# Performance work log

Hardware: AMD Instinct MI355X
Metric: run time of the kernel (lower is better)

The kernel has to match this reference:

```python
import jax, jax.numpy as jnp
import numpy as np

B, C, H, W = 2, 256, 80, 160
G, P, E = 8, 8, 2  # groups(heads), sampling points, ffn expansion
LN_EPS = 1e-5


def setup_inputs() -> dict:
    key = jax.random.key(0)
    ks = jax.random.split(key, 12)
    def n(k, shape, s=1.0):
        return jax.random.normal(k, shape, dtype=jnp.float32) * s
    return dict(
        feats=n(ks[0], (B, C, H, W)),
        feats_pos=n(ks[1], (B, C, H, W)),
        anchor_points=jax.random.uniform(ks[2], (B, H, W, 2), dtype=jnp.float32),
        value_W=n(ks[3], (C, C), 0.02), value_b=jnp.zeros((C,), jnp.float32),
        off_W=n(ks[4], (C, G * P * 2), 0.02), off_b=n(ks[5], (G * P * 2,), 0.02),
        attn_W=n(ks[6], (C, G * P), 0.02), attn_b=jnp.zeros((G * P,), jnp.float32),
        out_W=n(ks[7], (C, C), 0.02), out_b=jnp.zeros((C,), jnp.float32),
        ln1_g=jnp.ones((C,), jnp.float32), ln1_b=jnp.zeros((C,), jnp.float32),
        ln2_g=jnp.ones((C,), jnp.float32), ln2_b=jnp.zeros((C,), jnp.float32),
        ffn_w1=n(ks[8], (E * C, C), 0.02), ffn_b1=jnp.zeros((E * C,), jnp.float32),
        ffn_w2=n(ks[9], (C, E * C), 0.02), ffn_b2=jnp.zeros((C,), jnp.float32),
    )


def _layernorm(x, g, b):
    m = jnp.mean(x, axis=-1, keepdims=True)
    v = jnp.mean(jnp.square(x - m), axis=-1, keepdims=True)
    return (x - m) * jax.lax.rsqrt(v + LN_EPS) * g + b


def _bilinear_sample(value, px, py, h, w):
    # value: [b,G,HW,cg]; px,py: [b,G,P,HW] pixel coords (align_corners=False)
    x0 = jnp.floor(px); y0 = jnp.floor(py)
    wx1 = px - x0; wx0 = 1.0 - wx1
    wy1 = py - y0; wy0 = 1.0 - wy1
    vexp = value[:, :, None, :, :]  # [b,G,1,HW,cg]
    def gather(xi, yi):
        valid = ((xi >= 0) & (xi < w) & (yi >= 0) & (yi < h)).astype(value.dtype)
        xc = jnp.clip(xi, 0, w - 1).astype(jnp.int32)
        yc = jnp.clip(yi, 0, h - 1).astype(jnp.int32)
        idx = yc * w + xc  # [b,G,P,HW]
        v = jnp.take_along_axis(vexp, idx[..., None], axis=3)  # [b,G,P,HW,cg]
        return v * valid[..., None]
    return (gather(x0, y0) * (wx0 * wy0)[..., None]
            + gather(x0 + 1, y0) * (wx1 * wy0)[..., None]
            + gather(x0, y0 + 1) * (wx0 * wy1)[..., None]
            + gather(x0 + 1, y0 + 1) * (wx1 * wy1)[..., None])


def reference(feats, feats_pos, anchor_points,
              value_W, value_b, off_W, off_b, attn_W, attn_b, out_W, out_b,
              ln1_g, ln1_b, ln2_g, ln2_b, ffn_w1, ffn_b1, ffn_w2, ffn_b2):
    b, c, h, w = feats.shape
    hw = h * w
    cg = c // G
    x = feats + feats_pos                              # residual input (pos-encoded)
    q = x.reshape(b, c, hw).transpose(0, 2, 1)         # [b,HW,c]
    # deformable attention
    val = (q @ value_W + value_b).reshape(b, hw, G, cg).transpose(0, 2, 1, 3)   # [b,G,HW,cg]
    off = (q @ off_W + off_b).reshape(b, hw, G, P, 2).transpose(0, 2, 3, 1, 4)  # [b,G,P,HW,2]
    attn = jax.nn.softmax((q @ attn_W + attn_b).reshape(b, hw, G, P)
                          .transpose(0, 2, 3, 1), axis=2)                        # [b,G,P,HW]
    anchor = anchor_points.reshape(b, hw, 2)[:, None, None, :, :]               # [b,1,1,HW,2]
    loc = anchor + off / jnp.array([w, h], dtype=off.dtype)                     # normalized xy
    px = loc[..., 0] * w - 0.5
    py = loc[..., 1] * h - 0.5
    sampled = _bilinear_sample(val, px, py, h, w)                               # [b,G,P,HW,cg]
    agg = jnp.einsum('bgpn,bgpnc->bngc', attn, sampled).reshape(b, hw, c)
    upd = agg @ out_W + out_b
    # residual + LN1
    y = _layernorm(q + upd, ln1_g, ln1_b)
    # conv1x1 - SiLU - conv1x1 FFN + residual + LN2
    ffn = jax.nn.silu(y @ ffn_w1.T + ffn_b1) @ ffn_w2.T + ffn_b2
    y = _layernorm(y + ffn, ln2_g, ln2_b)
    return y.transpose(0, 2, 1).reshape(b, c, h, w)
```

## Files before the change

kernel.cpp:

```cpp
#include <hip/hip_runtime.h>
#include <hip/hip_bf16.h>
#include <math.h>
#include <stdint.h>

#define B_ 2
#define C_ 256
#define H_ 80
#define W_ 160
#define HW_ (H_*W_)
#define NTOK (B_*HW_)
#define G_ 8
#define P_ 8
#define NQKV 448
#define NQKVP 512

typedef __bf16 bf16;
typedef __attribute__((ext_vector_type(8))) __bf16 bf16x8;
typedef __attribute__((ext_vector_type(4))) float f32x4;

__device__ __forceinline__ void gload_lds16(const void* g, void* l) {
  __builtin_amdgcn_global_load_lds(
      (__attribute__((address_space(1))) void*)g,
      (__attribute__((address_space(3))) void*)l,
      16, 0, 0);
}

__global__ __launch_bounds__(256)
void prep_weights(const float* __restrict__ vW, const float* __restrict__ vb,
                  const float* __restrict__ oW, const float* __restrict__ ob,
                  const float* __restrict__ aW, const float* __restrict__ ab,
                  const float* __restrict__ outW,
                  const float* __restrict__ w1, const float* __restrict__ w2,
                  bf16* __restrict__ wqkv, float* __restrict__ bqkv,
                  bf16* __restrict__ woutt, bf16* __restrict__ w1b, bf16* __restrict__ w2b)
{
  int i = blockIdx.x * 256 + threadIdx.x;
  if (i < NQKVP*256) {
    int nn = i >> 8, k = i & 255;
    float w;
    if (nn < 256)      w = vW[k*256 + nn];
    else if (nn < 384) w = oW[k*128 + (nn-256)];
    else if (nn < 448) w = aW[k*64  + (nn-384)];
    else               w = 0.f;
    wqkv[i] = (bf16)w;
  }
  int j = i - NQKVP*256;
  if (j >= 0 && j < 256*256) {
    int nn = j >> 8, k = j & 255;
    woutt[j] = (bf16)outW[k*256 + nn];
  }
  int j2 = i - (NQKVP*256 + 256*256);
  if (j2 >= 0 && j2 < 512*256) w1b[j2] = (bf16)w1[j2];
  int j3 = i - (NQKVP*256 + 256*256 + 512*256);
  if (j3 >= 0 && j3 < 256*512) w2b[j3] = (bf16)w2[j3];
  int j4 = i - (NQKVP*256 + 256*256 + 512*256 + 256*512);
  if (j4 >= 0 && j4 < NQKVP) {
    float bv;
    if (j4 < 256)      bv = vb[j4];
    else if (j4 < 384) bv = ob[j4-256];
    else if (j4 < 448) bv = ab[j4-384];
    else               bv = 0.f;
    bqkv[j4] = bv;
  }
}

__global__ __launch_bounds__(256)
void qprep_kernel(const float* __restrict__ f, const float* __restrict__ fp,
                  bf16* __restrict__ qb)
{
  __shared__ float lt[64][65];
  const int tid = threadIdx.x;
  const int n0 = blockIdx.x * 64;
  const int c0 = blockIdx.y * 64;
  const int b  = blockIdx.z;
#pragma unroll
  for (int i = 0; i < 16; ++i) {
    int cl = i*4 + (tid >> 6), nl = tid & 63;
    size_t gi = ((size_t)(b*C_ + c0 + cl))*HW_ + n0 + nl;
    lt[cl][nl] = f[gi] + fp[gi];
  }
  __syncthreads();
#pragma unroll
  for (int i = 0; i < 16; ++i) {
    int nl = i*4 + (tid >> 6), cl = tid & 63;
    size_t qi = ((size_t)(b*HW_ + n0 + nl))*C_ + c0 + cl;
    qb[qi] = (bf16)lt[cl][nl];
  }
}

template<int EPI, int KTOT>
__global__ __launch_bounds__(256)
void gemm_kernel(const bf16* __restrict__ A, const bf16* __restrict__ Bt,
                 const float* __restrict__ bias,
                 void* __restrict__ out0, float* __restrict__ out1,
                 float* __restrict__ out2)
{
  __shared__ bf16 lA[128*64];
  __shared__ bf16 lB[128*64];
  const int tid  = threadIdx.x;
  const int wave = tid >> 6, lane = tid & 63;
  const int m0 = blockIdx.x * 128, n0 = blockIdx.y * 128;
  const int wm = wave >> 1, wn = wave & 1;
  const int fr = lane & 15;
  const int fq = lane >> 4;
  f32x4 acc[4][4] = {};

  for (int kc = 0; kc < KTOT/64; ++kc) {
    if (kc) __syncthreads();
#pragma unroll
    for (int it = 0; it < 4; ++it) {
      int chunk = it*256 + tid;
      int row = chunk >> 3, cb = chunk & 7;
      int ksw = ((cb ^ (row & 7)) << 3);
      gload_lds16(A  + (size_t)(m0+row)*KTOT + kc*64 + ksw,
                  (char*)lA + it*4096 + wave*1024);
      gload_lds16(Bt + (size_t)(n0+row)*KTOT + kc*64 + ksw,
                  (char*)lB + it*4096 + wave*1024);
    }
    __syncthreads();
#pragma unroll
    for (int ks = 0; ks < 2; ++ks) {
      bf16x8 af[4], bg[4];
#pragma unroll
      for (int i = 0; i < 4; ++i) {
        int ar = wm*64 + i*16 + fr;
        af[i] = *(const bf16x8*)&lA[ar*64 + (((ks*4 + fq) ^ (ar & 7)) << 3)];
        int br = wn*64 + i*16 + fr;
        bg[i] = *(const bf16x8*)&lB[br*64 + (((ks*4 + fq) ^ (br & 7)) << 3)];
      }
#pragma unroll
      for (int mi = 0; mi < 4; ++mi)
#pragma unroll
        for (int ni = 0; ni < 4; ++ni)
          acc[mi][ni] = __builtin_amdgcn_mfma_f32_16x16x32_bf16(af[mi], bg[ni], acc[mi][ni], 0, 0, 0);
    }
  }

#pragma unroll
  for (int mi = 0; mi < 4; ++mi)
#pragma unroll
  for (int ni = 0; ni < 4; ++ni)
#pragma unroll
  for (int r = 0; r < 4; ++r) {
    int row = m0 + wm*64 + mi*16 + fq*4 + r;
    int col = n0 + wn*64 + ni*16 + fr;
    float v = acc[mi][ni][r] + bias[col];
    if (EPI == 0) {
      if (col < 256) {
        int g = col >> 5, ch = col & 31;
        int b = row >= HW_ ? 1 : 0;
        int n = row - b*HW_;
        ((bf16*)out0)[(((size_t)(b*G_ + g))*HW_ + n)*32 + ch] = (bf16)v;
      }
      else if (col < 384) out1[(size_t)row*128 + (col-256)] = v;
      else if (col < 448) out2[(size_t)row*64  + (col-384)] = v;
    } else {
      float s = v / (1.0f + __expf(-v));
      ((bf16*)out0)[(size_t)row*512 + col] = (bf16)s;
    }
  }
}

template<int KTOT, bool NCHW_OUT>
__global__ __launch_bounds__(512)
void gemm_ln_kernel(const bf16* __restrict__ A, const bf16* __restrict__ Bt,
                    const float* __restrict__ bias, const bf16* __restrict__ res,
                    const float* __restrict__ gg, const float* __restrict__ bb,
                    bf16* __restrict__ yb, float* __restrict__ outf)
{
  __shared__ __align__(16) char smem[49152];
  bf16* lA = (bf16*)smem;
  bf16* lB = (bf16*)(smem + 16384);
  float (*lt)[132] = (float(*)[132])smem;
  __shared__ float2 red[128][4];
  const int tid  = threadIdx.x;
  const int wave = tid >> 6, lane = tid & 63;
  const int m0 = blockIdx.x * 128;
  const int wm = wave >> 2, wn = wave & 3;
  const int fr = lane & 15;
  const int fq = lane >> 4;
  f32x4 acc[4][4] = {};

  for (int kc = 0; kc < KTOT/64; ++kc) {
    if (kc) __syncthreads();
#pragma unroll
    for (int it = 0; it < 2; ++it) {
      int chunk = it*512 + tid;
      int row = chunk >> 3, cb = chunk & 7;
      int ksw = ((cb ^ (row & 7)) << 3);
      gload_lds16(A + (size_t)(m0+row)*KTOT + kc*64 + ksw,
                  (char*)lA + it*8192 + wave*1024);
    }
#pragma unroll
    for (int it = 0; it < 4; ++it) {
      int chunk = it*512 + tid;
      int row = chunk >> 3, cb = chunk & 7;
      int ksw = ((cb ^ (row & 7)) << 3);
      gload_lds16(Bt + (size_t)row*KTOT + kc*64 + ksw,
                  (char*)lB + it*8192 + wave*1024);
    }
    __syncthreads();
#pragma unroll
    for (int ks = 0; ks < 2; ++ks) {
      bf16x8 af[4], bg[4];
#pragma unroll
      for (int i = 0; i < 4; ++i) {
        int ar = wm*64 + i*16 + fr;
        af[i] = *(const bf16x8*)&lA[ar*64 + (((ks*4 + fq) ^ (ar & 7)) << 3)];
        int br = wn*64 + i*16 + fr;
        bg[i] = *(const bf16x8*)&lB[br*64 + (((ks*4 + fq) ^ (br & 7)) << 3)];
      }
#pragma unroll
      for (int mi = 0; mi < 4; ++mi)
#pragma unroll
        for (int ni = 0; ni < 4; ++ni)
          acc[mi][ni] = __builtin_amdgcn_mfma_f32_16x16x32_bf16(af[mi], bg[ni], acc[mi][ni], 0, 0, 0);
    }
  }

  float gcol[4], bcol[4];
#pragma unroll
  for (int ni = 0; ni < 4; ++ni) {
    int col = wn*64 + ni*16 + fr;
    gcol[ni] = gg[col]; bcol[ni] = bb[col];
  }
#pragma unroll
  for (int mi = 0; mi < 4; ++mi)
#pragma unroll
  for (int r = 0; r < 4; ++r) {
    int rowl = wm*64 + mi*16 + fq*4 + r;
    size_t rowg = (size_t)(m0 + rowl);
    float s = 0.f, q = 0.f;
#pragma unroll
    for (int ni = 0; ni < 4; ++ni) {
      int col = wn*64 + ni*16 + fr;
      float v = acc[mi][ni][r] + bias[col] + (float)res[rowg*256 + col];
      acc[mi][ni][r] = v;
      s += v; q += v*v;
    }
#pragma unroll
    for (int o = 1; o < 16; o <<= 1) { s += __shfl_xor(s, o, 64); q += __shfl_xor(q, o, 64); }
    if (fr == 0) red[rowl][wn] = make_float2(s, q);
  }
  __syncthreads();
#pragma unroll
  for (int mi = 0; mi < 4; ++mi)
#pragma unroll
  for (int r = 0; r < 4; ++r) {
    int rowl = wm*64 + mi*16 + fq*4 + r;
    float s = 0.f, q = 0.f;
#pragma unroll
    for (int k = 0; k < 4; ++k) { float2 p = red[rowl][k]; s += p.x; q += p.y; }
    const float mean = s * (1.f/256.f);
    const float var  = q * (1.f/256.f) - mean*mean;
    const float rs   = rsqrtf(var + 1e-5f);
#pragma unroll
    for (int ni = 0; ni < 4; ++ni)
      acc[mi][ni][r] = (acc[mi][ni][r] - mean)*rs*gcol[ni] + bcol[ni];
  }

  if constexpr (!NCHW_OUT) {
#pragma unroll
    for (int mi = 0; mi < 4; ++mi)
#pragma unroll
    for (int ni = 0; ni < 4; ++ni)
#pragma unroll
    for (int r = 0; r < 4; ++r) {
      size_t rowg = (size_t)(m0 + wm*64 + mi*16 + fq*4 + r);
      int col = wn*64 + ni*16 + fr;
      yb[rowg*256 + col] = (bf16)acc[mi][ni][r];
    }
  } else {
    const int bq = m0 / HW_;
    const int n0 = m0 % HW_;
    __syncthreads();
#pragma unroll
    for (int ch = 0; ch < 4; ++ch) {
      if (ch) __syncthreads();
      if (wn == ch) {
#pragma unroll
        for (int mi = 0; mi < 4; ++mi)
#pragma unroll
        for (int ni = 0; ni < 4; ++ni)
#pragma unroll
        for (int r = 0; r < 4; ++r)
          lt[ni*16 + fr][wm*64 + mi*16 + fq*4 + r] = acc[mi][ni][r];
      }
      __syncthreads();
#pragma unroll
      for (int j = 0; j < 4; ++j) {
        int flat = j*2048 + tid*4;
        int cl = flat >> 7, tk = flat & 127;
        float4 v4 = *(const float4*)&lt[cl][tk];
        *(float4*)&outf[((size_t)(bq*C_ + ch*64 + cl))*HW_ + n0 + tk] = v4;
      }
    }
  }
}

__global__ __launch_bounds__(256)
void sample_kernel(const bf16* __restrict__ val, const float* __restrict__ off,
                   const float* __restrict__ attnl, const float* __restrict__ anchors,
                   bf16* __restrict__ agg)
{
  const int tid  = threadIdx.x;
  const int lane = tid & 63;
  const int wv   = tid >> 6;
  const int c8   = lane & 3;
  const int bid  = blockIdx.x;
  const int g    = bid & 7;
  const int chunk= bid >> 3;
  const int t    = chunk*64 + wv*16 + (lane >> 2);
  const int b    = (t >= HW_) ? 1 : 0;

  const float2 anc = *(const float2*)(anchors + (size_t)t*2);
  const float ax = anc.x * W_ - 0.5f;
  const float ay = anc.y * H_ - 0.5f;

  const float4 l0 = *(const float4*)(attnl + (size_t)t*64 + g*8);
  const float4 l1 = *(const float4*)(attnl + (size_t)t*64 + g*8 + 4);
  float l[8] = {l0.x, l0.y, l0.z, l0.w, l1.x, l1.y, l1.z, l1.w};
  float mx = l[0];
#pragma unroll
  for (int p = 1; p < 8; ++p) mx = fmaxf(mx, l[p]);
  float s = 0.f;
#pragma unroll
  for (int p = 0; p < 8; ++p) { l[p] = __expf(l[p] - mx); s += l[p]; }
  const float inv = 1.f / s;

  const float4* opv = (const float4*)(off + (size_t)t*128 + g*16);
  const float4 o0 = opv[0], o1 = opv[1], o2 = opv[2], o3 = opv[3];
  const float ox[8] = {o0.x, o0.z, o1.x, o1.z, o2.x, o2.z, o3.x, o3.z};
  const float oy[8] = {o0.y, o0.w, o1.y, o1.w, o2.y, o2.w, o3.y, o3.w};

  const bf16* vb = val + ((size_t)(b*G_ + g)*HW_)*32 + c8*8;

  float a[8] = {};
#pragma unroll
  for (int p = 0; p < 8; ++p) {
    const float px = ax + ox[p], py = ay + oy[p];
    const float x0f = floorf(px), y0f = floorf(py);
    const int x0 = (int)x0f, y0 = (int)y0f;
    const float wx1 = px - x0f, wx0 = 1.f - wx1;
    const float wy1 = py - y0f, wy0 = 1.f - wy1;
    const float ap = l[p] * inv;
    float w00 = ap*wx0*wy0, w10 = ap*wx1*wy0, w01 = ap*wx0*wy1, w11 = ap*wx1*wy1;
    const bool vx0 = (unsigned)x0 < W_, vx1 = (unsigned)(x0+1) < W_;
    const bool vy0 = (unsigned)y0 < H_, vy1 = (unsigned)(y0+1) < H_;
    w00 = (vx0 && vy0) ? w00 : 0.f;  w10 = (vx1 && vy0) ? w10 : 0.f;
    w01 = (vx0 && vy1) ? w01 : 0.f;  w11 = (vx1 && vy1) ? w11 : 0.f;
    const int xc0 = min(max(x0, 0), W_-1),   xc1 = min(max(x0+1, 0), W_-1);
    const int yc0 = min(max(y0, 0), H_-1),   yc1 = min(max(y0+1, 0), H_-1);
    const bf16x8 v00 = *(const bf16x8*)(vb + (size_t)(yc0*W_ + xc0)*32);
    const bf16x8 v10 = *(const bf16x8*)(vb + (size_t)(yc0*W_ + xc1)*32);
    const bf16x8 v01 = *(const bf16x8*)(vb + (size_t)(yc1*W_ + xc0)*32);
    const bf16x8 v11 = *(const bf16x8*)(vb + (size_t)(yc1*W_ + xc1)*32);
#pragma unroll
    for (int c = 0; c < 8; ++c)
      a[c] += w00*(float)v00[c] + w10*(float)v10[c]
            + w01*(float)v01[c] + w11*(float)v11[c];
  }
  bf16 r[8];
#pragma unroll
  for (int c = 0; c < 8; ++c) r[c] = (bf16)a[c];
  *(bf16x8*)(agg + (size_t)t*256 + g*32 + c8*8) = *(bf16x8*)r;
}

extern "C" void kernel_launch(void* const* d_in, const int* in_sizes, int n_in,
                              void* d_out, int out_size, void* d_ws, size_t ws_size,
                              hipStream_t stream)
{
  const float* feats   = (const float*)d_in[0];
  const float* featsp  = (const float*)d_in[1];
  const float* anchors = (const float*)d_in[2];
  const float* value_W = (const float*)d_in[3];
  const float* value_b = (const float*)d_in[4];
  const float* off_W   = (const float*)d_in[5];
  const float* off_b   = (const float*)d_in[6];
  const float* attn_W  = (const float*)d_in[7];
  const float* attn_b  = (const float*)d_in[8];
  const float* out_W   = (const float*)d_in[9];
  const float* out_b   = (const float*)d_in[10];
  const float* ln1_g   = (const float*)d_in[11];
  const float* ln1_b   = (const float*)d_in[12];
  const float* ln2_g   = (const float*)d_in[13];
  const float* ln2_b   = (const float*)d_in[14];
  const float* w1      = (const float*)d_in[15];
  const float* b1      = (const float*)d_in[16];
  const float* w2      = (const float*)d_in[17];
  const float* b2      = (const float*)d_in[18];
  float* out = (float*)d_out;

  char* ws = (char*)d_ws;
  size_t cur = 0;
  auto alloc = [&](size_t bytes) -> char* {
    char* p = ws + cur;
    cur += (bytes + 255) & ~(size_t)255;
    return p;
  };
  bf16*  wqkv  = (bf16*) alloc((size_t)NQKVP*256*2);
  bf16*  woutt = (bf16*) alloc((size_t)256*256*2);
  bf16*  w1b   = (bf16*) alloc((size_t)512*256*2);
  bf16*  w2b   = (bf16*) alloc((size_t)256*512*2);
  float* bqkv  = (float*)alloc((size_t)NQKVP*4);
  bf16*  qb    = (bf16*) alloc((size_t)NTOK*256*2);
  bf16*  valb  = (bf16*) alloc((size_t)NTOK*256*2);
  float* offv  = (float*)alloc((size_t)NTOK*128*4);
  float* attnl = (float*)alloc((size_t)NTOK*64*4);
  bf16*  aggb  = (bf16*) alloc((size_t)NTOK*256*2);
  bf16*  y1b   = (bf16*) alloc((size_t)NTOK*256*2);
  bf16*  hb    = (bf16*) alloc((size_t)NTOK*512*2);

  prep_weights<<<(NQKVP*256 + 256*256 + 512*256 + 256*512 + NQKVP + 255)/256, 256, 0, stream>>>(
      value_W, value_b, off_W, off_b, attn_W, attn_b, out_W, w1, w2,
      wqkv, bqkv, woutt, w1b, w2b);

  qprep_kernel<<<dim3(HW_/64, C_/64, B_), 256, 0, stream>>>(feats, featsp, qb);

  gemm_kernel<0, 256><<<dim3(NTOK/128, NQKVP/128), 256, 0, stream>>>(
      qb, wqkv, bqkv, valb, offv, attnl);

  sample_kernel<<<NTOK/8, 256, 0, stream>>>(valb, offv, attnl, anchors, aggb);

  gemm_ln_kernel<256, false><<<NTOK/128, 512, 0, stream>>>(
      aggb, woutt, out_b, qb, ln1_g, ln1_b, y1b, nullptr);

  gemm_kernel<2, 256><<<dim3(NTOK/128, 512/128), 256, 0, stream>>>(
      y1b, w1b, b1, hb, nullptr, nullptr);

  gemm_ln_kernel<512, true><<<NTOK/128, 512, 0, stream>>>(
      hb, w2b, b2, y1b, ln2_g, ln2_b, nullptr, out);
}
```

Baseline: 145.3 us.

## Fuse FFN up-projection, SiLU, down-projection and LN2 into one kernel

Result: faster. 141.5 us (-2.6%).

```diff
diff --git a/kernel.cpp b/kernel.cpp
--- a/kernel.cpp
+++ b/kernel.cpp
@@ -154,24 +154,19 @@
       }
       else if (col < 384) out1[(size_t)row*128 + (col-256)] = v;
       else if (col < 448) out2[(size_t)row*64  + (col-384)] = v;
-    } else {
-      float s = v / (1.0f + __expf(-v));
-      ((bf16*)out0)[(size_t)row*512 + col] = (bf16)s;
-    }
-  }
-}
-
-template<int KTOT, bool NCHW_OUT>
+    }
+  }
+}
+
 __global__ __launch_bounds__(512)
 void gemm_ln_kernel(const bf16* __restrict__ A, const bf16* __restrict__ Bt,
                     const float* __restrict__ bias, const bf16* __restrict__ res,
                     const float* __restrict__ gg, const float* __restrict__ bb,
-                    bf16* __restrict__ yb, float* __restrict__ outf)
+                    bf16* __restrict__ yb)
 {
   __shared__ __align__(16) char smem[49152];
   bf16* lA = (bf16*)smem;
   bf16* lB = (bf16*)(smem + 16384);
-  float (*lt)[132] = (float(*)[132])smem;
   __shared__ float2 red[128][4];
   const int tid  = threadIdx.x;
   const int wave = tid >> 6, lane = tid & 63;
@@ -181,14 +176,14 @@
   const int fq = lane >> 4;
   f32x4 acc[4][4] = {};
 
-  for (int kc = 0; kc < KTOT/64; ++kc) {
+  for (int kc = 0; kc < 256/64; ++kc) {
     if (kc) __syncthreads();
 #pragma unroll
     for (int it = 0; it < 2; ++it) {
       int chunk = it*512 + tid;
       int row = chunk >> 3, cb = chunk & 7;
       int ksw = ((cb ^ (row & 7)) << 3);
-      gload_lds16(A + (size_t)(m0+row)*KTOT + kc*64 + ksw,
+      gload_lds16(A + (size_t)(m0+row)*256 + kc*64 + ksw,
                   (char*)lA + it*8192 + wave*1024);
     }
 #pragma unroll
@@ -196,7 +191,7 @@
       int chunk = it*512 + tid;
       int row = chunk >> 3, cb = chunk & 7;
       int ksw = ((cb ^ (row & 7)) << 3);
-      gload_lds16(Bt + (size_t)row*KTOT + kc*64 + ksw,
+      gload_lds16(Bt + (size_t)row*256 + kc*64 + ksw,
                   (char*)lB + it*8192 + wave*1024);
     }
     __syncthreads();
@@ -248,6 +243,7 @@
 #pragma unroll
   for (int r = 0; r < 4; ++r) {
     int rowl = wm*64 + mi*16 + fq*4 + r;
+    size_t rowg = (size_t)(m0 + rowl);
     float s = 0.f, q = 0.f;
 #pragma unroll
     for (int k = 0; k < 4; ++k) { float2 p = red[rowl][k]; s += p.x; q += p.y; }
@@ -255,45 +251,183 @@
     const float var  = q * (1.f/256.f) - mean*mean;
     const float rs   = rsqrtf(var + 1e-5f);
 #pragma unroll
+    for (int ni = 0; ni < 4; ++ni) {
+      int col = wn*64 + ni*16 + fr;
+      float y = (acc[mi][ni][r] - mean)*rs*gcol[ni] + bcol[ni];
+      yb[rowg*256 + col] = (bf16)y;
+    }
+  }
+}
+
+__global__ __launch_bounds__(512)
+void ffn_kernel(const bf16* __restrict__ y1b, const bf16* __restrict__ w1b,
+                const float* __restrict__ b1, const bf16* __restrict__ w2b,
+                const float* __restrict__ b2,
+                const float* __restrict__ gg, const float* __restrict__ bb,
+                float* __restrict__ outf)
+{
+  __shared__ __align__(16) char smem[131072];
+  bf16* yA  = (bf16*)smem;
+  bf16* hA  = (bf16*)(smem + 65536);
+  bf16* bst = (bf16*)(smem + 98304);
+  float (*lt)[132] = (float(*)[132])smem;
+  __shared__ float2 red[128][4];
+  const int tid  = threadIdx.x;
+  const int wave = tid >> 6, lane = tid & 63;
+  const int m0 = blockIdx.x * 128;
+  const int fr = lane & 15, fq = lane >> 4;
+  const int wm1 = wave >> 1, wn1 = wave & 1;
+  const int wm = wave >> 2,  wn = wave & 3;
+
+#pragma unroll
+  for (int it = 0; it < 8; ++it) {
+    int chunk = it*512 + tid;
+    int row = chunk >> 5, cb = chunk & 31;
+    gload_lds16(y1b + (size_t)(m0+row)*256 + ((cb ^ (row&7))<<3),
+                (char*)yA + it*8192 + wave*1024);
+  }
+  f32x4 acc2[4][4] = {};
+  __syncthreads();
+
+  for (int nc = 0; nc < 4; ++nc) {
+    f32x4 acc1[2][4] = {};
+    for (int kc = 0; kc < 4; ++kc) {
+#pragma unroll
+      for (int it = 0; it < 2; ++it) {
+        int chunk = it*512 + tid;
+        int row = chunk >> 3, cb = chunk & 7;
+        gload_lds16(w1b + (size_t)(nc*128+row)*256 + kc*64 + ((cb ^ (row&7))<<3),
+                    (char*)bst + it*8192 + wave*1024);
+      }
+      __syncthreads();
+#pragma unroll
+      for (int ks = 0; ks < 2; ++ks) {
+        bf16x8 af[2], bg[4];
+#pragma unroll
+        for (int i = 0; i < 2; ++i) {
+          int ar = wm1*32 + i*16 + fr;
+          af[i] = *(const bf16x8*)&yA[ar*256 + (((kc*8 + ks*4 + fq) ^ (ar&7))<<3)];
+        }
+#pragma unroll
+        for (int i = 0; i < 4; ++i) {
+          int br = wn1*64 + i*16 + fr;
+          bg[i] = *(const bf16x8*)&bst[br*64 + (((ks*4 + fq) ^ (br&7))<<3)];
+        }
+#pragma unroll
+        for (int mi = 0; mi < 2; ++mi)
+#pragma unroll
+          for (int ni = 0; ni < 4; ++ni)
+            acc1[mi][ni] = __builtin_amdgcn_mfma_f32_16x16x32_bf16(af[mi], bg[ni], acc1[mi][ni], 0,0,0);
+      }
+      __syncthreads();
+    }
+#pragma unroll
+    for (int mi = 0; mi < 2; ++mi)
+#pragma unroll
     for (int ni = 0; ni < 4; ++ni)
-      acc[mi][ni][r] = (acc[mi][ni][r] - mean)*rs*gcol[ni] + bcol[ni];
-  }
-
-  if constexpr (!NCHW_OUT) {
-#pragma unroll
-    for (int mi = 0; mi < 4; ++mi)
+#pragma unroll
+    for (int r = 0; r < 4; ++r) {
+      int row = wm1*32 + mi*16 + fq*4 + r;
+      int col = wn1*64 + ni*16 + fr;
+      float v = acc1[mi][ni][r] + b1[nc*128 + col];
+      float s = v / (1.0f + __expf(-v));
+      hA[row*128 + (((col>>3) ^ (row&7))<<3) + (col&7)] = (bf16)s;
+    }
+    __syncthreads();
+    for (int kc = 0; kc < 2; ++kc) {
+#pragma unroll
+      for (int it = 0; it < 4; ++it) {
+        int chunk = it*512 + tid;
+        int row = chunk >> 3, cb = chunk & 7;
+        gload_lds16(w2b + (size_t)row*512 + nc*128 + kc*64 + ((cb ^ (row&7))<<3),
+                    (char*)bst + it*8192 + wave*1024);
+      }
+      __syncthreads();
+#pragma unroll
+      for (int ks = 0; ks < 2; ++ks) {
+        bf16x8 af[4], bg[4];
+#pragma unroll
+        for (int i = 0; i < 4; ++i) {
+          int ar = wm*64 + i*16 + fr;
+          af[i] = *(const bf16x8*)&hA[ar*128 + (((kc*8 + ks*4 + fq) ^ (ar&7))<<3)];
+        }
+#pragma unroll
+        for (int i = 0; i < 4; ++i) {
+          int br = wn*64 + i*16 + fr;
+          bg[i] = *(const bf16x8*)&bst[br*64 + (((ks*4 + fq) ^ (br&7))<<3)];
+        }
+#pragma unroll
+        for (int mi = 0; mi < 4; ++mi)
+#pragma unroll
+          for (int ni = 0; ni < 4; ++ni)
+            acc2[mi][ni] = __builtin_amdgcn_mfma_f32_16x16x32_bf16(af[mi], bg[ni], acc2[mi][ni], 0,0,0);
+      }
+      __syncthreads();
+    }
+  }
+
+  float gcol[4], bcol[4];
+#pragma unroll
+  for (int ni = 0; ni < 4; ++ni) {
+    int col = wn*64 + ni*16 + fr;
+    gcol[ni] = gg[col]; bcol[ni] = bb[col];
+  }
+#pragma unroll
+  for (int mi = 0; mi < 4; ++mi)
+#pragma unroll
+  for (int r = 0; r < 4; ++r) {
+    int rowl = wm*64 + mi*16 + fq*4 + r;
+    size_t rowg = (size_t)(m0 + rowl);
+    float s = 0.f, q = 0.f;
+#pragma unroll
+    for (int ni = 0; ni < 4; ++ni) {
+      int col = wn*64 + ni*16 + fr;
+      float v = acc2[mi][ni][r] + b2[col] + (float)y1b[rowg*256 + col];
+      acc2[mi][ni][r] = v;
+      s += v; q += v*v;
+    }
+#pragma unroll
+    for (int o = 1; o < 16; o <<= 1) { s += __shfl_xor(s, o, 64); q += __shfl_xor(q, o, 64); }
+    if (fr == 0) red[rowl][wn] = make_float2(s, q);
+  }
+  __syncthreads();
+#pragma unroll
+  for (int mi = 0; mi < 4; ++mi)
+#pragma unroll
+  for (int r = 0; r < 4; ++r) {
+    int rowl = wm*64 + mi*16 + fq*4 + r;
+    float s = 0.f, q = 0.f;
+#pragma unroll
+    for (int k = 0; k < 4; ++k) { float2 p = red[rowl][k]; s += p.x; q += p.y; }
+    const float mean = s * (1.f/256.f);
+    const float var  = q * (1.f/256.f) - mean*mean;
+    const float rs   = rsqrtf(var + 1e-5f);
 #pragma unroll
     for (int ni = 0; ni < 4; ++ni)
-#pragma unroll
-    for (int r = 0; r < 4; ++r) {
-      size_t rowg = (size_t)(m0 + wm*64 + mi*16 + fq*4 + r);
-      int col = wn*64 + ni*16 + fr;
-      yb[rowg*256 + col] = (bf16)acc[mi][ni][r];
-    }
-  } else {
-    const int bq = m0 / HW_;
-    const int n0 = m0 % HW_;
+      acc2[mi][ni][r] = (acc2[mi][ni][r] - mean)*rs*gcol[ni] + bcol[ni];
+  }
+  const int bq = m0 / HW_;
+  const int n0 = m0 % HW_;
+  __syncthreads();
+#pragma unroll
+  for (int ch = 0; ch < 4; ++ch) {
+    if (ch) __syncthreads();
+    if (wn == ch) {
+#pragma unroll
+      for (int mi = 0; mi < 4; ++mi)
+#pragma unroll
+      for (int ni = 0; ni < 4; ++ni)
+#pragma unroll
+      for (int r = 0; r < 4; ++r)
+        lt[ni*16 + fr][wm*64 + mi*16 + fq*4 + r] = acc2[mi][ni][r];
+    }
     __syncthreads();
 #pragma unroll
-    for (int ch = 0; ch < 4; ++ch) {
-      if (ch) __syncthreads();
-      if (wn == ch) {
-#pragma unroll
-        for (int mi = 0; mi < 4; ++mi)
-#pragma unroll
-        for (int ni = 0; ni < 4; ++ni)
-#pragma unroll
-        for (int r = 0; r < 4; ++r)
-          lt[ni*16 + fr][wm*64 + mi*16 + fq*4 + r] = acc[mi][ni][r];
-      }
-      __syncthreads();
-#pragma unroll
-      for (int j = 0; j < 4; ++j) {
-        int flat = j*2048 + tid*4;
-        int cl = flat >> 7, tk = flat & 127;
-        float4 v4 = *(const float4*)&lt[cl][tk];
-        *(float4*)&outf[((size_t)(bq*C_ + ch*64 + cl))*HW_ + n0 + tk] = v4;
-      }
+    for (int j = 0; j < 4; ++j) {
+      int flat = j*2048 + tid*4;
+      int cl = flat >> 7, tk = flat & 127;
+      float4 v4 = *(const float4*)&lt[cl][tk];
+      *(float4*)&outf[((size_t)(bq*C_ + ch*64 + cl))*HW_ + n0 + tk] = v4;
     }
   }
 }
@@ -409,7 +543,6 @@
   float* attnl = (float*)alloc((size_t)NTOK*64*4);
   bf16*  aggb  = (bf16*) alloc((size_t)NTOK*256*2);
   bf16*  y1b   = (bf16*) alloc((size_t)NTOK*256*2);
-  bf16*  hb    = (bf16*) alloc((size_t)NTOK*512*2);
 
   prep_weights<<<(NQKVP*256 + 256*256 + 512*256 + 256*512 + NQKVP + 255)/256, 256, 0, stream>>>(
       value_W, value_b, off_W, off_b, attn_W, attn_b, out_W, w1, w2,
@@ -422,12 +555,9 @@
 
   sample_kernel<<<NTOK/8, 256, 0, stream>>>(valb, offv, attnl, anchors, aggb);
 
-  gemm_ln_kernel<256, false><<<NTOK/128, 512, 0, stream>>>(
-      aggb, woutt, out_b, qb, ln1_g, ln1_b, y1b, nullptr);
-
-  gemm_kernel<2, 256><<<dim3(NTOK/128, 512/128), 256, 0, stream>>>(
-      y1b, w1b, b1, hb, nullptr, nullptr);
-
-  gemm_ln_kernel<512, true><<<NTOK/128, 512, 0, stream>>>(
-      hb, w2b, b2, y1b, ln2_g, ln2_b, nullptr, out);
-}
+  gemm_ln_kernel<<<NTOK/128, 512, 0, stream>>>(
+      aggb, woutt, out_b, qb, ln1_g, ln1_b, y1b);
+
+  ffn_kernel<<<NTOK/128, 512, 0, stream>>>(
+      y1b, w1b, b1, w2b, b2, ln2_g, ln2_b, out);
+}
```
